# Kernel tuning notes

Hardware: AMD Instinct MI355X
Metric: run time of the kernel (lower is better)

## Reference

```python
import jax, jax.numpy as jnp
import numpy as np

DEC_HIDDEN = 512


def setup_inputs() -> dict:
    key = jax.random.key(0)
    k1, k2, k3, k4 = jax.random.split(key, 4)
    B, S, DEC, ENC2 = 32, 2048, 512, 1024
    s = jax.random.normal(k1, (1, B, DEC), dtype=jnp.float32)
    enc_output = jax.random.normal(k2, (B, S, ENC2), dtype=jnp.float32)
    # nn.Linear weights: attn [dec_hidden, enc_hidden*2 + dec_hidden], v [1, dec_hidden]
    W_attn = jax.random.normal(k3, (DEC, DEC + ENC2), dtype=jnp.float32) * (1.0 / np.sqrt(DEC + ENC2))
    W_v = jax.random.normal(k4, (1, DEC), dtype=jnp.float32) * (1.0 / np.sqrt(DEC))
    return {"s": s, "enc_output": enc_output, "W_attn": W_attn, "W_v": W_v}


def reference(s, enc_output, W_attn, W_v):
    # s: [1, B, D] -> [B, D]; enc_output: [B, S, 2E]
    s = jnp.squeeze(s, axis=0)
    dec = s.shape[-1]
    # torch.cat((s_repeated, enc_output), dim=2) @ W_attn.T, computed without
    # materializing the repeat/concat: split W_attn by column blocks.
    W_s = W_attn[:, :dec]       # [D, D]   (columns matching s)
    W_e = W_attn[:, dec:]       # [D, 2E]  (columns matching enc_output)
    # energy: [B, S, D]
    energy = jnp.tanh(
        jnp.einsum('bd,hd->bh', s, W_s)[:, None, :]
        + jnp.einsum('bse,he->bsh', enc_output, W_e)
    )
    # atten: [B, S]
    atten = jnp.einsum('bsh,h->bs', energy, W_v[0])
    soft_attn_weights = jax.nn.softmax(atten, axis=1)
    # context: [B, 2E]
    context = jnp.einsum('bs,bse->be', soft_attn_weights, enc_output)
    return (context, soft_attn_weights)
```

## Files before the change

### kernel.cpp

```cpp
#include <hip/hip_runtime.h>
#include <hip/hip_bf16.h>


typedef __attribute__((ext_vector_type(8))) short bf16x8;
typedef __attribute__((ext_vector_type(4))) float f32x4;
typedef __attribute__((address_space(3))) unsigned lds_u32;
typedef const __attribute__((address_space(1))) unsigned g_u32;

static __device__ __forceinline__ unsigned short f2bf(float f) {
    union { float f; unsigned u; } v; v.f = f;
    unsigned r = (v.u + 0x7fffu + ((v.u >> 16) & 1u)) >> 16;
    return (unsigned short)r;
}

static __device__ __forceinline__ unsigned pk2(float x, float y) {
    union { __hip_bfloat162 h; unsigned u; } c;
    c.h = __float22bfloat162_rn(make_float2(x, y));
    return c.u;
}

static __device__ __forceinline__ float fast_tanh(float x) {
    return 1.0f - 2.0f / (__expf(2.0f * x) + 1.0f);
}

__global__ __launch_bounds__(256) void prep_sw(const float* __restrict__ s,
                                               const float* __restrict__ Wat,
                                               float* __restrict__ sW) {
    int id = blockIdx.x * 256 + threadIdx.x;
    int b = id >> 9, h = id & 511;
    const float4* wr = (const float4*)(Wat + (size_t)h * 1536);
    const float4* sr = (const float4*)(s + (size_t)b * 512);
    float acc = 0.f;
#pragma unroll 8
    for (int i = 0; i < 128; ++i) {
        float4 w = wr[i], sv = sr[i];
        acc += w.x * sv.x + w.y * sv.y + w.z * sv.z + w.w * sv.w;
    }
    sW[id] = acc;
}

__global__ __launch_bounds__(256) void prep_weB(const float* __restrict__ Wat,
                                                unsigned short* __restrict__ WebfB) {
    int tid = blockIdx.x * 256 + threadIdx.x;
    int lane = tid & 63;
    int g = tid >> 6;
    int nf = g & 3, kk = (g >> 2) & 1, i = (g >> 3) & 15, w = g >> 7;
    int col = w * 64 + nf * 16 + (lane & 15);
    int k0 = i * 64 + kk * 32 + (lane >> 4) * 8;
    const float* src = Wat + (size_t)col * 1536 + 512 + k0;
    float4 w0 = *(const float4*)src;
    float4 w1 = *(const float4*)(src + 4);
    union { unsigned short us[8]; int4 v; } p;
    p.us[0] = f2bf(w0.x); p.us[1] = f2bf(w0.y); p.us[2] = f2bf(w0.z); p.us[3] = f2bf(w0.w);
    p.us[4] = f2bf(w1.x); p.us[5] = f2bf(w1.y); p.us[6] = f2bf(w1.z); p.us[7] = f2bf(w1.w);
    *(int4*)(WebfB + (size_t)tid * 8) = p.v;
}

__global__ __launch_bounds__(512) void energy_kernel(
    const float* __restrict__ enc, const unsigned short* __restrict__ WebfB,
    const float* __restrict__ sW, const float* __restrict__ Wv,
    float* __restrict__ atten) {
    __shared__ __align__(16) float lA[2][4096];
    __shared__ float lred[8][64];

    const int t = threadIdx.x;
    const int lane = t & 63;
    const int wave = t >> 6;
    const int m0 = blockIdx.x * 64;
    const int b = m0 >> 11;
    const int l15 = lane & 15;
    const int lkg = lane >> 4;
    const int n0 = wave * 64;

    const int r0 = wave * 8 + (lane >> 4);
    const int r1 = r0 + 4;
    const int cl0 = l15 ^ (r0 & 7);
    const int cl1 = l15 ^ (r1 & 7);
    const float* g0 = enc + (size_t)(m0 + r0) * 1024 + cl0 * 4;
    const float* g1 = enc + (size_t)(m0 + r1) * 1024 + cl1 * 4;
    const int ld0 = (wave * 2 + 0) * 256;
    const int ld1 = (wave * 2 + 1) * 256;

    const unsigned short* wB = WebfB + (size_t)wave * 65536 + lane * 8;

    f32x4 acc[4][4];
#pragma unroll
    for (int mf = 0; mf < 4; ++mf)
#pragma unroll
        for (int nf = 0; nf < 4; ++nf) acc[mf][nf] = (f32x4){0.f, 0.f, 0.f, 0.f};

    __builtin_amdgcn_global_load_lds((g_u32*)g0, (lds_u32*)&lA[0][ld0], 16, 0, 0);
    __builtin_amdgcn_global_load_lds((g_u32*)g1, (lds_u32*)&lA[0][ld1], 16, 0, 0);
    __syncthreads();

    for (int i = 0; i < 16; ++i) {
        const int cur = i & 1;
        bf16x8 bfr[2][4];
#pragma unroll
        for (int kk = 0; kk < 2; ++kk)
#pragma unroll
            for (int nf = 0; nf < 4; ++nf)
                bfr[kk][nf] = *(const bf16x8*)(wB + (((i * 2 + kk) * 4 + nf) << 9));
        __builtin_amdgcn_sched_barrier(0);
        if (i < 15) {
            __builtin_amdgcn_global_load_lds((g_u32*)(g0 + (i + 1) * 64),
                                             (lds_u32*)&lA[cur ^ 1][ld0], 16, 0, 0);
            __builtin_amdgcn_global_load_lds((g_u32*)(g1 + (i + 1) * 64),
                                             (lds_u32*)&lA[cur ^ 1][ld1], 16, 0, 0);
        }
        __builtin_amdgcn_sched_barrier(0);
        const float* lbuf = lA[cur];
#pragma unroll
        for (int kk = 0; kk < 2; ++kk) {
            const int c0 = kk * 8 + lkg * 2;
#pragma unroll
            for (int mf = 0; mf < 4; ++mf) {
                const int r = mf * 16 + l15;
                const int r7 = r & 7;
                float4 a0 = *(const float4*)&lbuf[r * 64 + ((c0 ^ r7) << 2)];
                float4 a1 = *(const float4*)&lbuf[r * 64 + (((c0 + 1) ^ r7) << 2)];
                union { unsigned u[4]; bf16x8 v; } af;
                af.u[0] = pk2(a0.x, a0.y); af.u[1] = pk2(a0.z, a0.w);
                af.u[2] = pk2(a1.x, a1.y); af.u[3] = pk2(a1.z, a1.w);
#pragma unroll
                for (int nf = 0; nf < 4; ++nf)
                    acc[mf][nf] = __builtin_amdgcn_mfma_f32_16x16x32_bf16(
                        af.v, bfr[kk][nf], acc[mf][nf], 0, 0, 0);
            }
        }
        __syncthreads();
    }

    float sWv[4], wvv[4];
#pragma unroll
    for (int nf = 0; nf < 4; ++nf) {
        int col = n0 + nf * 16 + l15;
        sWv[nf] = sW[(b << 9) + col];
        wvv[nf] = Wv[col];
    }
    float pa[4][4];
#pragma unroll
    for (int mf = 0; mf < 4; ++mf) {
#pragma unroll
        for (int r = 0; r < 4; ++r) pa[mf][r] = 0.f;
#pragma unroll
        for (int nf = 0; nf < 4; ++nf)
#pragma unroll
            for (int r = 0; r < 4; ++r)
                pa[mf][r] += fast_tanh(acc[mf][nf][r] + sWv[nf]) * wvv[nf];
    }
#pragma unroll
    for (int m = 1; m < 16; m <<= 1)
#pragma unroll
        for (int mf = 0; mf < 4; ++mf)
#pragma unroll
            for (int r = 0; r < 4; ++r)
                pa[mf][r] += __shfl_xor(pa[mf][r], m, 64);

    if (l15 == 0) {
#pragma unroll
        for (int mf = 0; mf < 4; ++mf)
#pragma unroll
            for (int r = 0; r < 4; ++r)
                lred[wave][mf * 16 + lkg * 4 + r] = pa[mf][r];
    }
    __syncthreads();
    if (t < 64) {
        float ssum = 0.f;
#pragma unroll
        for (int w = 0; w < 8; ++w) ssum += lred[w][t];
        atten[m0 + t] = ssum;
    }
}

__global__ __launch_bounds__(256) void softmax_kernel(const float* __restrict__ atten,
                                                      float* __restrict__ out) {
    int b = blockIdx.x, t = threadIdx.x;
    const float* row = atten + b * 2048;
    float v[8];
#pragma unroll
    for (int i = 0; i < 8; ++i) v[i] = row[t + 256 * i];
    float mx = v[0];
#pragma unroll
    for (int i = 1; i < 8; ++i) mx = fmaxf(mx, v[i]);
#pragma unroll
    for (int m = 1; m < 64; m <<= 1) mx = fmaxf(mx, __shfl_xor(mx, m, 64));
    __shared__ float redm[4], reds[4];
    if ((t & 63) == 0) redm[t >> 6] = mx;
    __syncthreads();
    mx = fmaxf(fmaxf(redm[0], redm[1]), fmaxf(redm[2], redm[3]));
    float sum = 0.f;
#pragma unroll
    for (int i = 0; i < 8; ++i) { v[i] = __expf(v[i] - mx); sum += v[i]; }
#pragma unroll
    for (int m = 1; m < 64; m <<= 1) sum += __shfl_xor(sum, m, 64);
    if ((t & 63) == 0) reds[t >> 6] = sum;
    __syncthreads();
    sum = reds[0] + reds[1] + reds[2] + reds[3];
    float inv = 1.0f / sum;
    float* soft = out + 32768;
#pragma unroll
    for (int i = 0; i < 8; ++i) soft[b * 2048 + t + 256 * i] = v[i] * inv;
}

__global__ __launch_bounds__(256) void ctx_partial(const float* __restrict__ enc,
                                                   const float* __restrict__ soft,
                                                   float* __restrict__ part) {
    int blk = blockIdx.x;
    int b = blk >> 5, s0 = (blk & 31) * 64;
    int t = threadIdx.x;
    float4 a = {0.f, 0.f, 0.f, 0.f};
    const float* base = enc + ((size_t)(b * 2048 + s0)) * 1024 + t * 4;
    const float* sw = soft + b * 2048 + s0;
#pragma unroll 4
    for (int s = 0; s < 64; ++s) {
        float w = sw[s];
        float4 e = *(const float4*)(base + (size_t)s * 1024);
        a.x += w * e.x; a.y += w * e.y; a.z += w * e.z; a.w += w * e.w;
    }
    *(float4*)(part + (size_t)blk * 1024 + t * 4) = a;
}

__global__ __launch_bounds__(256) void ctx_reduce(const float* __restrict__ part,
                                                  float* __restrict__ ctx) {
    int id = blockIdx.x * 256 + threadIdx.x;
    int b = id >> 10, e = id & 1023;
    float s = 0.f;
#pragma unroll 8
    for (int c = 0; c < 32; ++c) s += part[((size_t)(b * 32 + c)) * 1024 + e];
    ctx[id] = s;
}

extern "C" void kernel_launch(void* const* d_in, const int* in_sizes, int n_in,
                              void* d_out, int out_size, void* d_ws, size_t ws_size,
                              hipStream_t stream) {
    const float* s   = (const float*)d_in[0];
    const float* enc = (const float*)d_in[1];
    const float* Wat = (const float*)d_in[2];
    const float* Wv  = (const float*)d_in[3];
    float* out = (float*)d_out;

    char* ws = (char*)d_ws;
    float* sW             = (float*)ws;
    unsigned short* WebfB = (unsigned short*)(ws + (64 << 10));
    float* atten          = (float*)(ws + (64 << 10) + (1 << 20));
    float* part           = (float*)(ws + (64 << 10) + (1 << 20) + (256 << 10));

    prep_sw<<<64, 256, 0, stream>>>(s, Wat, sW);
    prep_weB<<<256, 256, 0, stream>>>(Wat, WebfB);
    energy_kernel<<<1024, 512, 0, stream>>>(enc, WebfB, sW, Wv, atten);
    softmax_kernel<<<32, 256, 0, stream>>>(atten, out);
    ctx_partial<<<1024, 256, 0, stream>>>(enc, out + 32768, part);
    ctx_reduce<<<128, 256, 0, stream>>>(part, out);
}
```

Baseline: 182.6 us.

## Split energy GEMM N across blocks, triple-buffer LDS with explicit waitcnt pipeline

The energy kernel now runs 2048 blocks of 256 threads, each covering half of the hidden dimension, and combines the two halves with atomicAdd into a pre-zeroed atten buffer. The A tile is now triple-buffered, with hand-placed vmcnt waits and s_barrier, and B fragments are double-buffered in registers so global loads overlap MFMA compute. This means each enc tile is read twice, once per N-half, and an extra zero kernel is launched. In exchange it gets more blocks per CU and deeper prefetch.

```diff
diff --git a/kernel.cpp b/kernel.cpp
--- a/kernel.cpp
+++ b/kernel.cpp
@@ -6,6 +6,8 @@
 typedef __attribute__((ext_vector_type(4))) float f32x4;
 typedef __attribute__((address_space(3))) unsigned lds_u32;
 typedef const __attribute__((address_space(1))) unsigned g_u32;
+
+#define SB0() __builtin_amdgcn_sched_barrier(0)
 
 static __device__ __forceinline__ unsigned short f2bf(float f) {
     union { float f; unsigned u; } v; v.f = f;
@@ -56,32 +58,36 @@
     *(int4*)(WebfB + (size_t)tid * 8) = p.v;
 }
 
-__global__ __launch_bounds__(512) void energy_kernel(
+__global__ __launch_bounds__(256, 2) void energy_kernel(
     const float* __restrict__ enc, const unsigned short* __restrict__ WebfB,
     const float* __restrict__ sW, const float* __restrict__ Wv,
     float* __restrict__ atten) {
-    __shared__ __align__(16) float lA[2][4096];
-    __shared__ float lred[8][64];
+    __shared__ __align__(16) float lA[3][4096];
+    __shared__ float lred[4][64];
 
     const int t = threadIdx.x;
     const int lane = t & 63;
     const int wave = t >> 6;
-    const int m0 = blockIdx.x * 64;
+    const int bid = blockIdx.x;
+    const int m0 = (bid & 1023) * 64;
+    const int nh = bid >> 10;
     const int b = m0 >> 11;
     const int l15 = lane & 15;
     const int lkg = lane >> 4;
-    const int n0 = wave * 64;
-
-    const int r0 = wave * 8 + (lane >> 4);
-    const int r1 = r0 + 4;
-    const int cl0 = l15 ^ (r0 & 7);
-    const int cl1 = l15 ^ (r1 & 7);
-    const float* g0 = enc + (size_t)(m0 + r0) * 1024 + cl0 * 4;
-    const float* g1 = enc + (size_t)(m0 + r1) * 1024 + cl1 * 4;
-    const int ld0 = (wave * 2 + 0) * 256;
-    const int ld1 = (wave * 2 + 1) * 256;
-
-    const unsigned short* wB = WebfB + (size_t)wave * 65536 + lane * 8;
+    const int cg = nh * 4 + wave;
+    const int n0 = cg * 64;
+
+    const float* gsrc[4];
+    int ldoff[4];
+#pragma unroll
+    for (int q = 0; q < 4; ++q) {
+        int rq = wave * 16 + q * 4 + lkg;
+        int cl = l15 ^ (rq & 7);
+        gsrc[q] = enc + (size_t)(m0 + rq) * 1024 + cl * 4;
+        ldoff[q] = (wave * 16 + q * 4) * 64;
+    }
+
+    const unsigned short* wB = WebfB + (size_t)cg * 65536 + lane * 8;
 
     f32x4 acc[4][4];
 #pragma unroll
@@ -89,27 +95,20 @@
 #pragma unroll
         for (int nf = 0; nf < 4; ++nf) acc[mf][nf] = (f32x4){0.f, 0.f, 0.f, 0.f};
 
-    __builtin_amdgcn_global_load_lds((g_u32*)g0, (lds_u32*)&lA[0][ld0], 16, 0, 0);
-    __builtin_amdgcn_global_load_lds((g_u32*)g1, (lds_u32*)&lA[0][ld1], 16, 0, 0);
-    __syncthreads();
-
-    for (int i = 0; i < 16; ++i) {
-        const int cur = i & 1;
-        bf16x8 bfr[2][4];
+    auto stage = [&](int step, float* buf) {
+#pragma unroll
+        for (int q = 0; q < 4; ++q)
+            __builtin_amdgcn_global_load_lds((g_u32*)(gsrc[q] + step * 64),
+                                             (lds_u32*)(buf + ldoff[q]), 16, 0, 0);
+    };
+    auto loadB = [&](int step, bf16x8* bf) {
 #pragma unroll
         for (int kk = 0; kk < 2; ++kk)
 #pragma unroll
             for (int nf = 0; nf < 4; ++nf)
-                bfr[kk][nf] = *(const bf16x8*)(wB + (((i * 2 + kk) * 4 + nf) << 9));
-        __builtin_amdgcn_sched_barrier(0);
-        if (i < 15) {
-            __builtin_amdgcn_global_load_lds((g_u32*)(g0 + (i + 1) * 64),
-                                             (lds_u32*)&lA[cur ^ 1][ld0], 16, 0, 0);
-            __builtin_amdgcn_global_load_lds((g_u32*)(g1 + (i + 1) * 64),
-                                             (lds_u32*)&lA[cur ^ 1][ld1], 16, 0, 0);
-        }
-        __builtin_amdgcn_sched_barrier(0);
-        const float* lbuf = lA[cur];
+                bf[kk * 4 + nf] = *(const bf16x8*)(wB + (((step * 2 + kk) * 4 + nf) << 9));
+    };
+    auto compute = [&](const float* lbuf, const bf16x8* bf) {
 #pragma unroll
         for (int kk = 0; kk < 2; ++kk) {
             const int c0 = kk * 8 + lkg * 2;
@@ -125,11 +124,53 @@
 #pragma unroll
                 for (int nf = 0; nf < 4; ++nf)
                     acc[mf][nf] = __builtin_amdgcn_mfma_f32_16x16x32_bf16(
-                        af.v, bfr[kk][nf], acc[mf][nf], 0, 0, 0);
+                        af.v, bf[kk * 4 + nf], acc[mf][nf], 0, 0, 0);
             }
         }
-        __syncthreads();
-    }
+    };
+
+    float* p0 = (float*)lA[0];
+    float* p1 = (float*)lA[1];
+    float* p2 = (float*)lA[2];
+    bf16x8 bA[8], bB[8];
+
+    stage(0, p0);
+    loadB(0, bA);
+    stage(1, p1);
+
+#pragma unroll 1
+    for (int k = 0; k < 7; ++k) {
+        const int i = 2 * k;
+        asm volatile("s_waitcnt vmcnt(12)" ::: "memory");
+        SB0();
+        __builtin_amdgcn_s_barrier();
+        loadB(i + 1, bB);
+        SB0();
+        stage(i + 2, p2);
+        SB0();
+        compute(p0, bA);
+        { float* tp = p0; p0 = p1; p1 = p2; p2 = tp; }
+        asm volatile("s_waitcnt vmcnt(12)" ::: "memory");
+        SB0();
+        __builtin_amdgcn_s_barrier();
+        loadB(i + 2, bA);
+        SB0();
+        stage(i + 3, p2);
+        SB0();
+        compute(p0, bB);
+        { float* tp = p0; p0 = p1; p1 = p2; p2 = tp; }
+    }
+    asm volatile("s_waitcnt vmcnt(12)" ::: "memory");
+    SB0();
+    __builtin_amdgcn_s_barrier();
+    loadB(15, bB);
+    SB0();
+    compute(p0, bA);
+    { float* tp = p0; p0 = p1; p1 = p2; p2 = tp; }
+    asm volatile("s_waitcnt vmcnt(8)" ::: "memory");
+    SB0();
+    __builtin_amdgcn_s_barrier();
+    compute(p0, bB);
 
     float sWv[4], wvv[4];
 #pragma unroll
@@ -166,11 +207,13 @@
     }
     __syncthreads();
     if (t < 64) {
-        float ssum = 0.f;
-#pragma unroll
-        for (int w = 0; w < 8; ++w) ssum += lred[w][t];
-        atten[m0 + t] = ssum;
-    }
+        float ssum = lred[0][t] + lred[1][t] + lred[2][t] + lred[3][t];
+        atomicAdd(&atten[m0 + t], ssum);
+    }
+}
+
+__global__ __launch_bounds__(256) void zero_atten(float* __restrict__ atten) {
+    atten[blockIdx.x * 256 + threadIdx.x] = 0.f;
 }
 
 __global__ __launch_bounds__(256) void softmax_kernel(const float* __restrict__ atten,
@@ -248,7 +291,8 @@
 
     prep_sw<<<64, 256, 0, stream>>>(s, Wat, sW);
     prep_weB<<<256, 256, 0, stream>>>(Wat, WebfB);
-    energy_kernel<<<1024, 512, 0, stream>>>(enc, WebfB, sW, Wv, atten);
+    zero_atten<<<256, 256, 0, stream>>>(atten);
+    energy_kernel<<<2048, 256, 0, stream>>>(enc, WebfB, sW, Wv, atten);
     softmax_kernel<<<32, 256, 0, stream>>>(atten, out);
     ctx_partial<<<1024, 256, 0, stream>>>(enc, out + 32768, part);
     ctx_reduce<<<128, 256, 0, stream>>>(part, out);
```

Measured after the change: 195.9 us. 1.07x slower.

## Retile energy GEMM into 128x128 tiles with register-staged bf16 LDS

Applied to the files above, without the earlier changes.

The energy GEMM now uses 256-thread blocks, each computing a 128-row by 128-column tile, so the H dimension is split across four column tiles. Per-tile partial attention scores are written out and summed in the softmax kernel. The A operand is loaded from global memory into registers, converted to bf16 once, and written to LDS, which halves LDS footprint and removes the per-MFMA repacking. The cost is that enc is reread four times (once per column tile), and a block-index swizzle is added to keep those rereads in L2. The context partial kernel is also changed to cover 128 sequence positions per block, with fewer blocks and fewer partials to reduce.

```diff
diff --git a/kernel.cpp b/kernel.cpp
--- a/kernel.cpp
+++ b/kernel.cpp
@@ -4,8 +4,8 @@
 
 typedef __attribute__((ext_vector_type(8))) short bf16x8;
 typedef __attribute__((ext_vector_type(4))) float f32x4;
-typedef __attribute__((address_space(3))) unsigned lds_u32;
-typedef const __attribute__((address_space(1))) unsigned g_u32;
+
+#define SB0() __builtin_amdgcn_sched_barrier(0)
 
 static __device__ __forceinline__ unsigned short f2bf(float f) {
     union { float f; unsigned u; } v; v.f = f;
@@ -44,9 +44,9 @@
     int tid = blockIdx.x * 256 + threadIdx.x;
     int lane = tid & 63;
     int g = tid >> 6;
-    int nf = g & 3, kk = (g >> 2) & 1, i = (g >> 3) & 15, w = g >> 7;
-    int col = w * 64 + nf * 16 + (lane & 15);
-    int k0 = i * 64 + kk * 32 + (lane >> 4) * 8;
+    int nf = g & 7, step = (g >> 3) & 31, cg = g >> 8;
+    int col = cg * 128 + nf * 16 + (lane & 15);
+    int k0 = step * 32 + (lane >> 4) * 8;
     const float* src = Wat + (size_t)col * 1536 + 512 + k0;
     float4 w0 = *(const float4*)src;
     float4 w1 = *(const float4*)(src + 4);
@@ -56,32 +56,32 @@
     *(int4*)(WebfB + (size_t)tid * 8) = p.v;
 }
 
-__global__ __launch_bounds__(512) void energy_kernel(
+__global__ __launch_bounds__(256, 3) void energy_kernel(
     const float* __restrict__ enc, const unsigned short* __restrict__ WebfB,
     const float* __restrict__ sW, const float* __restrict__ Wv,
-    float* __restrict__ atten) {
-    __shared__ __align__(16) float lA[2][4096];
-    __shared__ float lred[8][64];
+    float* __restrict__ attpart) {
+    __shared__ __align__(16) unsigned short lA[2][8192];
+    __shared__ float lred[4][64];
 
     const int t = threadIdx.x;
     const int lane = t & 63;
     const int wave = t >> 6;
-    const int m0 = blockIdx.x * 64;
+    const int rg = wave >> 1;
+    const int cgw = wave & 1;
+    const int bid = blockIdx.x;
+    const int ct = (bid >> 3) & 3;
+    const int rt = ((bid >> 5) << 3) | (bid & 7);
+    const int m0 = rt * 128;
     const int b = m0 >> 11;
     const int l15 = lane & 15;
     const int lkg = lane >> 4;
-    const int n0 = wave * 64;
-
-    const int r0 = wave * 8 + (lane >> 4);
-    const int r1 = r0 + 4;
-    const int cl0 = l15 ^ (r0 & 7);
-    const int cl1 = l15 ^ (r1 & 7);
-    const float* g0 = enc + (size_t)(m0 + r0) * 1024 + cl0 * 4;
-    const float* g1 = enc + (size_t)(m0 + r1) * 1024 + cl1 * 4;
-    const int ld0 = (wave * 2 + 0) * 256;
-    const int ld1 = (wave * 2 + 1) * 256;
-
-    const unsigned short* wB = WebfB + (size_t)wave * 65536 + lane * 8;
+
+    const float* abase = enc + (size_t)m0 * 1024 + (t >> 4) * 1024 + (t & 15) * 4;
+    const int wlo = (t >> 4) * 128 + (((t & 15) * 8) ^ (((t >> 4) & 7) << 4));
+    const int rbase0 = (rg * 64 + l15) * 128 + ((lkg ^ (l15 & 7)) << 4);
+    const int rbase1 = rbase0 ^ 64;
+
+    const unsigned short* wB = WebfB + (size_t)ct * 131072 + lane * 8;
 
     f32x4 acc[4][4];
 #pragma unroll
@@ -89,52 +89,74 @@
 #pragma unroll
         for (int nf = 0; nf < 4; ++nf) acc[mf][nf] = (f32x4){0.f, 0.f, 0.f, 0.f};
 
-    __builtin_amdgcn_global_load_lds((g_u32*)g0, (lds_u32*)&lA[0][ld0], 16, 0, 0);
-    __builtin_amdgcn_global_load_lds((g_u32*)g1, (lds_u32*)&lA[0][ld1], 16, 0, 0);
-    __syncthreads();
-
-    for (int i = 0; i < 16; ++i) {
-        const int cur = i & 1;
-        bf16x8 bfr[2][4];
+    float4 areg[8];
+    auto load8 = [&](int step) {
+#pragma unroll
+        for (int q = 0; q < 8; ++q)
+            areg[q] = *(const float4*)(abase + q * 16384 + step * 64);
+    };
+    auto cvtwrite = [&](unsigned short* buf) {
+        char* base = (char*)buf + wlo;
+#pragma unroll
+        for (int q = 0; q < 8; ++q) {
+            uint2 w;
+            w.x = pk2(areg[q].x, areg[q].y);
+            w.y = pk2(areg[q].z, areg[q].w);
+            *(uint2*)(base + q * 2048) = w;
+        }
+    };
+    bf16x8 bfr[8];
+    auto loadB = [&](int i) {
 #pragma unroll
         for (int kk = 0; kk < 2; ++kk)
 #pragma unroll
             for (int nf = 0; nf < 4; ++nf)
-                bfr[kk][nf] = *(const bf16x8*)(wB + (((i * 2 + kk) * 4 + nf) << 9));
-        __builtin_amdgcn_sched_barrier(0);
-        if (i < 15) {
-            __builtin_amdgcn_global_load_lds((g_u32*)(g0 + (i + 1) * 64),
-                                             (lds_u32*)&lA[cur ^ 1][ld0], 16, 0, 0);
-            __builtin_amdgcn_global_load_lds((g_u32*)(g1 + (i + 1) * 64),
-                                             (lds_u32*)&lA[cur ^ 1][ld1], 16, 0, 0);
-        }
-        __builtin_amdgcn_sched_barrier(0);
-        const float* lbuf = lA[cur];
+                bfr[kk * 4 + nf] = *(const bf16x8*)(
+                    wB + (((size_t)((i * 2 + kk) * 8 + cgw * 4 + nf)) << 9));
+    };
+    auto compute = [&](const unsigned short* buf) {
 #pragma unroll
         for (int kk = 0; kk < 2; ++kk) {
-            const int c0 = kk * 8 + lkg * 2;
+            const int rb = kk ? rbase1 : rbase0;
 #pragma unroll
             for (int mf = 0; mf < 4; ++mf) {
-                const int r = mf * 16 + l15;
-                const int r7 = r & 7;
-                float4 a0 = *(const float4*)&lbuf[r * 64 + ((c0 ^ r7) << 2)];
-                float4 a1 = *(const float4*)&lbuf[r * 64 + (((c0 + 1) ^ r7) << 2)];
-                union { unsigned u[4]; bf16x8 v; } af;
-                af.u[0] = pk2(a0.x, a0.y); af.u[1] = pk2(a0.z, a0.w);
-                af.u[2] = pk2(a1.x, a1.y); af.u[3] = pk2(a1.z, a1.w);
+                bf16x8 af = *(const bf16x8*)((const char*)buf + rb + mf * 2048);
 #pragma unroll
                 for (int nf = 0; nf < 4; ++nf)
                     acc[mf][nf] = __builtin_amdgcn_mfma_f32_16x16x32_bf16(
-                        af.v, bfr[kk][nf], acc[mf][nf], 0, 0, 0);
+                        af, bfr[kk * 4 + nf], acc[mf][nf], 0, 0, 0);
             }
         }
-        __syncthreads();
+    };
+
+    unsigned short* cur = lA[0];
+    unsigned short* nxt = lA[1];
+
+    load8(0);
+    cvtwrite(cur);
+    load8(1);
+    asm volatile("s_waitcnt lgkmcnt(0)" ::: "memory");
+    __builtin_amdgcn_s_barrier();
+
+#pragma unroll 2
+    for (int i = 0; i < 16; ++i) {
+        loadB(i);
+        SB0();
+        if (i < 15) cvtwrite(nxt);
+        SB0();
+        if (i < 14) load8(i + 2);
+        SB0();
+        compute(cur);
+        asm volatile("s_waitcnt lgkmcnt(0)" ::: "memory");
+        SB0();
+        __builtin_amdgcn_s_barrier();
+        { unsigned short* tp = cur; cur = nxt; nxt = tp; }
     }
 
     float sWv[4], wvv[4];
 #pragma unroll
     for (int nf = 0; nf < 4; ++nf) {
-        int col = n0 + nf * 16 + l15;
+        int col = ct * 128 + cgw * 64 + nf * 16 + l15;
         sWv[nf] = sW[(b << 9) + col];
         wvv[nf] = Wv[col];
     }
@@ -165,21 +187,23 @@
                 lred[wave][mf * 16 + lkg * 4 + r] = pa[mf][r];
     }
     __syncthreads();
-    if (t < 64) {
-        float ssum = 0.f;
-#pragma unroll
-        for (int w = 0; w < 8; ++w) ssum += lred[w][t];
-        atten[m0 + t] = ssum;
-    }
-}
-
-__global__ __launch_bounds__(256) void softmax_kernel(const float* __restrict__ atten,
+    if (t < 128) {
+        int rgw = t >> 6, rl = t & 63;
+        attpart[(size_t)ct * 65536 + m0 + t] =
+            lred[rgw * 2 + 0][rl] + lred[rgw * 2 + 1][rl];
+    }
+}
+
+__global__ __launch_bounds__(256) void softmax_kernel(const float* __restrict__ attpart,
                                                       float* __restrict__ out) {
     int b = blockIdx.x, t = threadIdx.x;
-    const float* row = atten + b * 2048;
     float v[8];
 #pragma unroll
-    for (int i = 0; i < 8; ++i) v[i] = row[t + 256 * i];
+    for (int i = 0; i < 8; ++i) {
+        int idx = b * 2048 + t + 256 * i;
+        v[i] = ((attpart[idx] + attpart[65536 + idx]) + attpart[131072 + idx])
+               + attpart[196608 + idx];
+    }
     float mx = v[0];
 #pragma unroll
     for (int i = 1; i < 8; ++i) mx = fmaxf(mx, v[i]);
@@ -207,13 +231,13 @@
                                                    const float* __restrict__ soft,
                                                    float* __restrict__ part) {
     int blk = blockIdx.x;
-    int b = blk >> 5, s0 = (blk & 31) * 64;
+    int b = blk >> 4, s0 = (blk & 15) * 128;
     int t = threadIdx.x;
     float4 a = {0.f, 0.f, 0.f, 0.f};
     const float* base = enc + ((size_t)(b * 2048 + s0)) * 1024 + t * 4;
     const float* sw = soft + b * 2048 + s0;
 #pragma unroll 4
-    for (int s = 0; s < 64; ++s) {
+    for (int s = 0; s < 128; ++s) {
         float w = sw[s];
         float4 e = *(const float4*)(base + (size_t)s * 1024);
         a.x += w * e.x; a.y += w * e.y; a.z += w * e.z; a.w += w * e.w;
@@ -227,7 +251,7 @@
     int b = id >> 10, e = id & 1023;
     float s = 0.f;
 #pragma unroll 8
-    for (int c = 0; c < 32; ++c) s += part[((size_t)(b * 32 + c)) * 1024 + e];
+    for (int c = 0; c < 16; ++c) s += part[((size_t)(b * 16 + c)) * 1024 + e];
     ctx[id] = s;
 }
 
@@ -243,13 +267,13 @@
     char* ws = (char*)d_ws;
     float* sW             = (float*)ws;
     unsigned short* WebfB = (unsigned short*)(ws + (64 << 10));
-    float* atten          = (float*)(ws + (64 << 10) + (1 << 20));
-    float* part           = (float*)(ws + (64 << 10) + (1 << 20) + (256 << 10));
+    float* attpart        = (float*)(ws + (64 << 10) + (1 << 20));
+    float* part           = (float*)(ws + (64 << 10) + (2 << 20));
 
     prep_sw<<<64, 256, 0, stream>>>(s, Wat, sW);
     prep_weB<<<256, 256, 0, stream>>>(Wat, WebfB);
-    energy_kernel<<<1024, 512, 0, stream>>>(enc, WebfB, sW, Wv, atten);
-    softmax_kernel<<<32, 256, 0, stream>>>(atten, out);
-    ctx_partial<<<1024, 256, 0, stream>>>(enc, out + 32768, part);
+    energy_kernel<<<2048, 256, 0, stream>>>(enc, WebfB, sW, Wv, attpart);
+    softmax_kernel<<<32, 256, 0, stream>>>(attpart, out);
+    ctx_partial<<<512, 256, 0, stream>>>(enc, out + 32768, part);
     ctx_reduce<<<128, 256, 0, stream>>>(part, out);
 }
```

Result: faster. 178.1 us (-2.5%).
